# Kernel optimization log

Hardware: AMD Instinct MI355X
Metric: run time of the kernel (lower is better)

The kernel has to match this reference:

```python
import jax, jax.numpy as jnp
import numpy as np

SR = 16000
HOP = 256
MIN_F0 = 50.0
MAX_F0 = 500.0
MIN_PERIOD = SR // 500          # 32
MAX_PERIOD = SR // 50           # 320
FRAME_LEN = HOP * 2             # 512
LAG_END = min(MAX_PERIOD, FRAME_LEN // 2)  # 256 -> lags 32..255 (224 lags)


def setup_inputs() -> dict:
    key = jax.random.key(0)
    waveform = jax.random.normal(key, (64, 1, 163840), dtype=jnp.float32)
    return {"waveform": waveform}


def reference(waveform):
    B, C, T = waveform.shape
    x = waveform[:, 0, :]  # (B, T)
    pad = FRAME_LEN // 2
    xpad = jnp.pad(x, ((0, 0), (pad, pad)), mode='reflect')
    n_frames = (T + 2 * pad - FRAME_LEN) // HOP + 1  # = T//HOP + 1
    # frame extraction (equivalent to unfold(frame_length, hop))
    idx = np.arange(n_frames)[:, None] * HOP + np.arange(FRAME_LEN)[None, :]
    frames = xpad[:, idx]  # (B, F, L)
    # L2-normalize each frame
    norm = jnp.sqrt(jnp.sum(frames * frames, axis=-1, keepdims=True))
    xn = frames / (norm + 1e-8)
    # zero-pad right so xn[t] * xz[t+p] reproduces frame[:L-p] * frame[p:]
    xz = jnp.pad(xn, ((0, 0), (0, 0), (0, FRAME_LEN)))
    lags = jnp.arange(MIN_PERIOD, LAG_END)

    def step(carry, p):
        sl = jax.lax.dynamic_slice_in_dim(xz, p, FRAME_LEN, axis=-1)
        return carry, jnp.sum(xn * sl, axis=-1)  # (B, F)

    _, ac = jax.lax.scan(step, None, lags)  # (P, B, F)
    max_idx = jnp.argmax(ac, axis=0)  # (B, F)
    period = max_idx.astype(jnp.float32) + MIN_PERIOD
    f0 = SR / (period + 1e-8)
    return jnp.clip(f0, MIN_F0, MAX_F0)  # (B, F)
```

## Files before the change

kernel.cpp:

```cpp
#include <hip/hip_runtime.h>


#define SR_F 16000.0f
#define HOP 256
#define FRAME_LEN 512
#define PAD 256
#define T_LEN 163840
#define N_FRAMES 641
#define MIN_PERIOD 32
#define N_LAGS 224
#define FPB 4
#define GAP_B32 0.0625f

typedef _Float16 half8 __attribute__((ext_vector_type(8)));
typedef float floatx4 __attribute__((ext_vector_type(4)));

__device__ __forceinline__ int swz(int q) { return q ^ ((q >> 3) & 7); }

__device__ __forceinline__ unsigned int pkh(float a, float b) {
    unsigned short ha = __builtin_bit_cast(unsigned short, (_Float16)a);
    unsigned short hb = __builtin_bit_cast(unsigned short, (_Float16)b);
    return (unsigned int)ha | ((unsigned int)hb << 16);
}

__global__ __launch_bounds__(256, 4) void f0_kernel(const float* __restrict__ wav,
                                                    float* __restrict__ out) {
    __shared__ unsigned int yw[FPB][800];

    const int tid  = threadIdx.x;
    const int wv   = tid >> 6;
    const int lane = tid & 63;
    const int bf   = blockIdx.x * FPB + wv;
    const int b    = bf / N_FRAMES;
    const int f    = bf - b * N_FRAMES;
    const float* __restrict__ x = wav + (size_t)b * T_LEN;
    unsigned int* ye = yw[wv];
    unsigned int* yo = ye + 400;
    const int base = f * HOP - PAD;

    ye[lane] = 0u; yo[lane] = 0u;
    if (lane < 56) { ye[64 + lane] = 0u; yo[64 + lane] = 0u; }
    if (lane < 25) { ye[375 + lane] = 0u; yo[375 + lane] = 0u; }

    float qen = 0.0f;
    if (f != 0 && f != N_FRAMES - 1) {
        const float4* g4 = (const float4*)(x + base);
        float4 c1 = g4[lane];
        float4 c2 = g4[lane + 64];
        qen = c1.x*c1.x + c1.y*c1.y + c1.z*c1.z + c1.w*c1.w
            + c2.x*c2.x + c2.y*c2.y + c2.z*c2.z + c2.w*c2.w;
        unsigned int u10 = pkh(c1.x, c1.y), u11 = pkh(c1.z, c1.w);
        unsigned int u20 = pkh(c2.x, c2.y), u21 = pkh(c2.z, c2.w);
        ye[120 + 2*lane] = u10;  ye[121 + 2*lane] = u11;
        ye[248 + 2*lane] = u20;  ye[249 + 2*lane] = u21;
        unsigned int a  = __shfl(u10, (lane + 1) & 63);
        unsigned int bb = __shfl(u20, (lane + 1) & 63);
        unsigned int n1 = (lane == 63) ? bb : a;
        unsigned int n2 = (lane == 63) ? 0u : bb;
        yo[120 + 2*lane] = (u10 >> 16) | (u11 << 16);
        yo[121 + 2*lane] = (u11 >> 16) | (n1 << 16);
        yo[248 + 2*lane] = (u20 >> 16) | (u21 << 16);
        yo[249 + 2*lane] = (u21 >> 16) | (n2 << 16);
        if (lane == 0) yo[119] = u10 << 16;
    } else {
        for (int t = lane; t < FRAME_LEN; t += 64) {
            int idx = base + t;
            if (idx < 0) idx = -idx;
            if (idx >= T_LEN) idx = 2 * (T_LEN - 1) - idx;
            float v = x[idx];
            qen = __builtin_fmaf(v, v, qen);
            unsigned short h = __builtin_bit_cast(unsigned short, (_Float16)v);
            ((unsigned short*)ye)[240 + t] = h;
            ((unsigned short*)yo)[239 + t] = h;
        }
    }
    __threadfence_block();

    #pragma unroll
    for (int m = 1; m < 64; m <<= 1) qen += __shfl_xor(qen, m);

    const int qd = lane >> 4;
    const int nn = lane & 15;
    const int par = nn & 1;
    const unsigned int* yb = par ? yo : ye;
    const int wA0 = 120 + 4*qd - 8*nn;
    const int wB0 = 136 + 4*qd + ((nn - par) >> 1);

    floatx4 acc = {0.f, 0.f, 0.f, 0.f};
    #pragma unroll
    for (int c = 0; c < 16; ++c) {
        uint4 au = *(const uint4*)(ye + (wA0 + 16*c));
        const unsigned int* pb = yb + (wB0 + 16*c);
        uint4 bu;
        bu.x = pb[0]; bu.y = pb[1]; bu.z = pb[2]; bu.w = pb[3];
        half8 af = __builtin_bit_cast(half8, au);
        half8 bfv = __builtin_bit_cast(half8, bu);
        acc = __builtin_amdgcn_mfma_f32_16x16x32_f16(af, bfv, acc, 0, 0, 0);
    }

    float v1 = acc[0];
    int   i1 = 64*qd + nn;
    float v2 = -__builtin_inff();
    #pragma unroll
    for (int r = 1; r < 4; ++r) {
        float cv = (4*qd + r < 14) ? acc[r] : -__builtin_inff();
        bool take = (cv > v1);
        float lose = take ? v1 : cv;
        if (take) { v1 = cv; i1 = 64*qd + 16*r + nn; }
        v2 = fmaxf(v2, lose);
    }
    #pragma unroll
    for (int m = 1; m < 64; m <<= 1) {
        float ov1 = __shfl_xor(v1, m);
        float ov2 = __shfl_xor(v2, m);
        int   oi1 = __shfl_xor(i1, m);
        bool take = (ov1 > v1) || (ov1 == v1 && oi1 < i1);
        float lose = take ? v1 : ov1;
        if (take) { v1 = ov1; i1 = oi1; }
        v2 = fmaxf(fmaxf(v2, ov2), lose);
    }

    const float E1 = 9.765625e-4f * qen + 0.05f;
    if (v1 - v2 > 2.0f * E1) {
        if (lane == 0) {
            float period = (float)(i1 + MIN_PERIOD);
            float f0 = SR_F / (period + 1e-8f);
            out[bf] = fminf(fmaxf(f0, 50.0f), 500.0f);
        }
        return;
    }

    float* sw = (float*)ye;
    if (f != 0 && f != N_FRAMES - 1) {
        const float4* g4 = (const float4*)(x + base);
        ((float4*)sw)[swz(lane)]      = g4[lane];
        ((float4*)sw)[swz(lane + 64)] = g4[lane + 64];
        if (lane < 16) ((float4*)sw)[swz(lane + 128)] = make_float4(0.f,0.f,0.f,0.f);
    } else {
        for (int t = lane; t < FRAME_LEN; t += 64) {
            int idx = base + t;
            if (idx < 0) idx = -idx;
            if (idx >= T_LEN) idx = 2 * (T_LEN - 1) - idx;
            sw[(swz(t >> 2) << 2) | (t & 3)] = x[idx];
        }
        int t = FRAME_LEN + lane;
        sw[(swz(t >> 2) << 2) | (t & 3)] = 0.0f;
    }
    __threadfence_block();

    const float4* s4 = (const float4*)sw;
    const int seg = lane & 15;
    const bool s0 = (seg & 1), s1 = (seg & 2), s2 = (seg & 4), s3 = (seg & 8);

    float tot[4];
    #pragma unroll
    for (int r = 0; r < 4; ++r) {
        const int g  = (r << 2) + qd;
        const int p0 = MIN_PERIOD + (g << 4);
        float acc2[16];
        #pragma unroll
        for (int j = 0; j < 16; ++j) acc2[j] = 0.0f;
        if (g < 14) {
            const int n16 = (FRAME_LEN - p0 + 15) >> 4;
            #pragma unroll
            for (int k = 0; k < 2; ++k) {
                const int ch = seg + (k << 4);
                if (ch < n16) {
                    const int t  = ch << 4;
                    const int qa = t >> 2;
                    const int qw = (t + p0) >> 2;
                    float a[16], w[32];
                    #pragma unroll
                    for (int u = 0; u < 4; ++u) {
                        float4 v = s4[swz(qa + u)];
                        a[4*u+0]=v.x; a[4*u+1]=v.y; a[4*u+2]=v.z; a[4*u+3]=v.w;
                    }
                    #pragma unroll
                    for (int u = 0; u < 8; ++u) {
                        float4 v = s4[swz(qw + u)];
                        w[4*u+0]=v.x; w[4*u+1]=v.y; w[4*u+2]=v.z; w[4*u+3]=v.w;
                    }
                    #pragma unroll
                    for (int j = 0; j < 16; ++j) {
                        #pragma unroll
                        for (int i = 0; i < 16; ++i)
                            acc2[j] = __builtin_fmaf(a[i], w[i + j], acc2[j]);
                    }
                }
            }
        }
        float t8[8], t4[4], t2[2], total;
        #pragma unroll
        for (int i = 0; i < 8; ++i) {
            float lo = acc2[2*i], hi = acc2[2*i+1];
            float keep = s0 ? hi : lo, send = s0 ? lo : hi;
            t8[i] = keep + __shfl_xor(send, 1);
        }
        #pragma unroll
        for (int i = 0; i < 4; ++i) {
            float lo = t8[2*i], hi = t8[2*i+1];
            float keep = s1 ? hi : lo, send = s1 ? lo : hi;
            t4[i] = keep + __shfl_xor(send, 2);
        }
        #pragma unroll
        for (int i = 0; i < 2; ++i) {
            float lo = t4[2*i], hi = t4[2*i+1];
            float keep = s2 ? hi : lo, send = s2 ? lo : hi;
            t2[i] = keep + __shfl_xor(send, 4);
        }
        {
            float lo = t2[0], hi = t2[1];
            float keep = s3 ? hi : lo, send = s3 ? lo : hi;
            total = keep + __shfl_xor(send, 8);
        }
        tot[r] = ((r << 6) + lane < N_LAGS) ? total : -__builtin_inff();
    }

    float w1 = tot[0], w2 = -__builtin_inff();
    int   j1 = lane;
    #pragma unroll
    for (int r = 1; r < 4; ++r) {
        float c = tot[r];
        bool take = (c > w1);
        float lose = take ? w1 : c;
        if (take) { w1 = c; j1 = (r << 6) + lane; }
        w2 = fmaxf(w2, lose);
    }
    #pragma unroll
    for (int m = 1; m < 64; m <<= 1) {
        float ov1 = __shfl_xor(w1, m);
        float ov2 = __shfl_xor(w2, m);
        int   oi1 = __shfl_xor(j1, m);
        bool take = (ov1 > w1) || (ov1 == w1 && oi1 < j1);
        float lose = take ? w1 : ov1;
        if (take) { w1 = ov1; j1 = oi1; }
        w2 = fmaxf(fmaxf(w2, ov2), lose);
    }

    if (w1 - w2 > GAP_B32) {
        if (lane == 0) {
            float period = (float)(j1 + MIN_PERIOD);
            float f0 = SR_F / (period + 1e-8f);
            out[bf] = fminf(fmaxf(f0, 50.0f), 500.0f);
        }
        return;
    }

    double dtot[4];
    #pragma unroll
    for (int r = 0; r < 4; ++r) {
        const int g  = (r << 2) + qd;
        const int p0 = MIN_PERIOD + (g << 4);
        double dacc[16];
        #pragma unroll
        for (int j = 0; j < 16; ++j) dacc[j] = 0.0;
        if (g < 14) {
            const int n16 = (FRAME_LEN - p0 + 15) >> 4;
            #pragma unroll
            for (int k = 0; k < 2; ++k) {
                const int ch = seg + (k << 4);
                if (ch < n16) {
                    const int t  = ch << 4;
                    const int qa = t >> 2;
                    const int qw = (t + p0) >> 2;
                    float a[16], w[32];
                    #pragma unroll
                    for (int u = 0; u < 4; ++u) {
                        float4 v = s4[swz(qa + u)];
                        a[4*u+0]=v.x; a[4*u+1]=v.y; a[4*u+2]=v.z; a[4*u+3]=v.w;
                    }
                    #pragma unroll
                    for (int u = 0; u < 8; ++u) {
                        float4 v = s4[swz(qw + u)];
                        w[4*u+0]=v.x; w[4*u+1]=v.y; w[4*u+2]=v.z; w[4*u+3]=v.w;
                    }
                    #pragma unroll
                    for (int j = 0; j < 16; ++j) {
                        #pragma unroll
                        for (int i = 0; i < 16; ++i)
                            dacc[j] = fma((double)a[i], (double)w[i + j], dacc[j]);
                    }
                }
            }
        }
        double u8[8], u4[4], u2[2], dtotal;
        #pragma unroll
        for (int i = 0; i < 8; ++i) {
            double lo = dacc[2*i], hi = dacc[2*i+1];
            double keep = s0 ? hi : lo, send = s0 ? lo : hi;
            u8[i] = keep + __shfl_xor(send, 1);
        }
        #pragma unroll
        for (int i = 0; i < 4; ++i) {
            double lo = u8[2*i], hi = u8[2*i+1];
            double keep = s1 ? hi : lo, send = s1 ? lo : hi;
            u4[i] = keep + __shfl_xor(send, 2);
        }
        #pragma unroll
        for (int i = 0; i < 2; ++i) {
            double lo = u4[2*i], hi = u4[2*i+1];
            double keep = s2 ? hi : lo, send = s2 ? lo : hi;
            u2[i] = keep + __shfl_xor(send, 4);
        }
        {
            double lo = u2[0], hi = u2[1];
            double keep = s3 ? hi : lo, send = s3 ? lo : hi;
            dtotal = keep + __shfl_xor(send, 8);
        }
        dtot[r] = ((r << 6) + lane < N_LAGS) ? dtotal : -__builtin_inf();
    }
    double dv1 = dtot[0];
    int    di1 = lane;
    #pragma unroll
    for (int r = 1; r < 4; ++r) {
        double c = dtot[r];
        if (c > dv1) { dv1 = c; di1 = (r << 6) + lane; }
    }
    #pragma unroll
    for (int m = 1; m < 64; m <<= 1) {
        double o = __shfl_xor(dv1, m);
        int   oi = __shfl_xor(di1, m);
        if (o > dv1 || (o == dv1 && oi < di1)) { dv1 = o; di1 = oi; }
    }
    if (lane == 0) {
        float period = (float)(di1 + MIN_PERIOD);
        float f0 = SR_F / (period + 1e-8f);
        out[bf] = fminf(fmaxf(f0, 50.0f), 500.0f);
    }
}

extern "C" void kernel_launch(void* const* d_in, const int* in_sizes, int n_in,
                              void* d_out, int out_size, void* d_ws, size_t ws_size,
                              hipStream_t stream) {
    const float* wav = (const float*)d_in[0];
    float* out = (float*)d_out;
    const int n_blocks = (64 * N_FRAMES) / FPB;
    f0_kernel<<<n_blocks, 256, 0, stream>>>(wav, out);
}
```

Measured before the change: 150.2 us.

## Replace fp32 FMA fallback tier with split-fp16 MFMA correction tier

Removes the second-tier fp32 scalar-FMA autocorrelation and replaces it with a residual-corrected MFMA pass. The low-order fp16 remainder of each sample is stored in extra LDS buffers and two more MFMA sweeps (hi*lo and lo*hi) are added to the accumulator, with a tighter error bound deciding whether to accept the argmax before falling back to fp64. Block size also goes from 4 to 8 frames (512 threads) with doubled LDS per wave. This cuts the expensive fp32 FMA work for ambiguous frames, at the cost of more LDS use, which may lower occupancy, and reliance on the new error bound being correct.

```diff
diff --git a/kernel.cpp b/kernel.cpp
--- a/kernel.cpp
+++ b/kernel.cpp
@@ -9,8 +9,7 @@
 #define N_FRAMES 641
 #define MIN_PERIOD 32
 #define N_LAGS 224
-#define FPB 4
-#define GAP_B32 0.0625f
+#define FPB 8
 
 typedef _Float16 half8 __attribute__((ext_vector_type(8)));
 typedef float floatx4 __attribute__((ext_vector_type(4)));
@@ -23,9 +22,26 @@
     return (unsigned int)ha | ((unsigned int)hb << 16);
 }
 
-__global__ __launch_bounds__(256, 4) void f0_kernel(const float* __restrict__ wav,
+__device__ __forceinline__ void write_copies(unsigned int* e, unsigned int* o,
+                                             unsigned int u10, unsigned int u11,
+                                             unsigned int u20, unsigned int u21,
+                                             int lane) {
+    e[120 + 2*lane] = u10;  e[121 + 2*lane] = u11;
+    e[248 + 2*lane] = u20;  e[249 + 2*lane] = u21;
+    unsigned int a  = __shfl(u10, (lane + 1) & 63);
+    unsigned int bb = __shfl(u20, (lane + 1) & 63);
+    unsigned int n1 = (lane == 63) ? bb : a;
+    unsigned int n2 = (lane == 63) ? 0u : bb;
+    o[120 + 2*lane] = (u10 >> 16) | (u11 << 16);
+    o[121 + 2*lane] = (u11 >> 16) | (n1 << 16);
+    o[248 + 2*lane] = (u20 >> 16) | (u21 << 16);
+    o[249 + 2*lane] = (u21 >> 16) | (n2 << 16);
+    if (lane == 0) o[119] = u10 << 16;
+}
+
+__global__ __launch_bounds__(512, 4) void f0_kernel(const float* __restrict__ wav,
                                                     float* __restrict__ out) {
-    __shared__ unsigned int yw[FPB][800];
+    __shared__ unsigned int yw[FPB][1600];
 
     const int tid  = threadIdx.x;
     const int wv   = tid >> 6;
@@ -34,34 +50,26 @@
     const int b    = bf / N_FRAMES;
     const int f    = bf - b * N_FRAMES;
     const float* __restrict__ x = wav + (size_t)b * T_LEN;
-    unsigned int* ye = yw[wv];
-    unsigned int* yo = ye + 400;
+    unsigned int* ye  = yw[wv];
+    unsigned int* yo  = ye + 400;
+    unsigned int* le  = ye + 800;
+    unsigned int* loo = ye + 1200;
     const int base = f * HOP - PAD;
+    const bool fast = (f != 0 && f != N_FRAMES - 1);
 
     ye[lane] = 0u; yo[lane] = 0u;
     if (lane < 56) { ye[64 + lane] = 0u; yo[64 + lane] = 0u; }
     if (lane < 25) { ye[375 + lane] = 0u; yo[375 + lane] = 0u; }
 
     float qen = 0.0f;
-    if (f != 0 && f != N_FRAMES - 1) {
+    if (fast) {
         const float4* g4 = (const float4*)(x + base);
         float4 c1 = g4[lane];
         float4 c2 = g4[lane + 64];
         qen = c1.x*c1.x + c1.y*c1.y + c1.z*c1.z + c1.w*c1.w
             + c2.x*c2.x + c2.y*c2.y + c2.z*c2.z + c2.w*c2.w;
-        unsigned int u10 = pkh(c1.x, c1.y), u11 = pkh(c1.z, c1.w);
-        unsigned int u20 = pkh(c2.x, c2.y), u21 = pkh(c2.z, c2.w);
-        ye[120 + 2*lane] = u10;  ye[121 + 2*lane] = u11;
-        ye[248 + 2*lane] = u20;  ye[249 + 2*lane] = u21;
-        unsigned int a  = __shfl(u10, (lane + 1) & 63);
-        unsigned int bb = __shfl(u20, (lane + 1) & 63);
-        unsigned int n1 = (lane == 63) ? bb : a;
-        unsigned int n2 = (lane == 63) ? 0u : bb;
-        yo[120 + 2*lane] = (u10 >> 16) | (u11 << 16);
-        yo[121 + 2*lane] = (u11 >> 16) | (n1 << 16);
-        yo[248 + 2*lane] = (u20 >> 16) | (u21 << 16);
-        yo[249 + 2*lane] = (u21 >> 16) | (n2 << 16);
-        if (lane == 0) yo[119] = u10 << 16;
+        write_copies(ye, yo, pkh(c1.x, c1.y), pkh(c1.z, c1.w),
+                             pkh(c2.x, c2.y), pkh(c2.z, c2.w), lane);
     } else {
         for (int t = lane; t < FRAME_LEN; t += 64) {
             int idx = base + t;
@@ -82,7 +90,7 @@
     const int qd = lane >> 4;
     const int nn = lane & 15;
     const int par = nn & 1;
-    const unsigned int* yb = par ? yo : ye;
+    const unsigned int* ybh = par ? yo : ye;
     const int wA0 = 120 + 4*qd - 8*nn;
     const int wB0 = 136 + 4*qd + ((nn - par) >> 1);
 
@@ -90,12 +98,11 @@
     #pragma unroll
     for (int c = 0; c < 16; ++c) {
         uint4 au = *(const uint4*)(ye + (wA0 + 16*c));
-        const unsigned int* pb = yb + (wB0 + 16*c);
-        uint4 bu;
-        bu.x = pb[0]; bu.y = pb[1]; bu.z = pb[2]; bu.w = pb[3];
-        half8 af = __builtin_bit_cast(half8, au);
-        half8 bfv = __builtin_bit_cast(half8, bu);
-        acc = __builtin_amdgcn_mfma_f32_16x16x32_f16(af, bfv, acc, 0, 0, 0);
+        const unsigned int* pb = ybh + (wB0 + 16*c);
+        uint4 bu; bu.x = pb[0]; bu.y = pb[1]; bu.z = pb[2]; bu.w = pb[3];
+        acc = __builtin_amdgcn_mfma_f32_16x16x32_f16(
+            __builtin_bit_cast(half8, au), __builtin_bit_cast(half8, bu),
+            acc, 0, 0, 0);
     }
 
     float v1 = acc[0];
@@ -130,8 +137,89 @@
         return;
     }
 
+    le[lane] = 0u; loo[lane] = 0u;
+    if (lane < 56) { le[64 + lane] = 0u; loo[64 + lane] = 0u; }
+    if (lane < 25) { le[375 + lane] = 0u; loo[375 + lane] = 0u; }
+    if (fast) {
+        const float4* g4 = (const float4*)(x + base);
+        float4 c1 = g4[lane];
+        float4 c2 = g4[lane + 64];
+        float l0 = c1.x - (float)(_Float16)c1.x;
+        float l1 = c1.y - (float)(_Float16)c1.y;
+        float l2 = c1.z - (float)(_Float16)c1.z;
+        float l3 = c1.w - (float)(_Float16)c1.w;
+        float l4 = c2.x - (float)(_Float16)c2.x;
+        float l5 = c2.y - (float)(_Float16)c2.y;
+        float l6 = c2.z - (float)(_Float16)c2.z;
+        float l7 = c2.w - (float)(_Float16)c2.w;
+        write_copies(le, loo, pkh(l0, l1), pkh(l2, l3),
+                              pkh(l4, l5), pkh(l6, l7), lane);
+    } else {
+        for (int t = lane; t < FRAME_LEN; t += 64) {
+            int idx = base + t;
+            if (idx < 0) idx = -idx;
+            if (idx >= T_LEN) idx = 2 * (T_LEN - 1) - idx;
+            float v = x[idx];
+            float l = v - (float)(_Float16)v;
+            unsigned short h = __builtin_bit_cast(unsigned short, (_Float16)l);
+            ((unsigned short*)le)[240 + t] = h;
+            ((unsigned short*)loo)[239 + t] = h;
+        }
+    }
+    __threadfence_block();
+
+    const unsigned int* ybl = par ? loo : le;
+    #pragma unroll
+    for (int c = 0; c < 16; ++c) {
+        uint4 au = *(const uint4*)(ye + (wA0 + 16*c));
+        const unsigned int* pb = ybl + (wB0 + 16*c);
+        uint4 bu; bu.x = pb[0]; bu.y = pb[1]; bu.z = pb[2]; bu.w = pb[3];
+        acc = __builtin_amdgcn_mfma_f32_16x16x32_f16(
+            __builtin_bit_cast(half8, au), __builtin_bit_cast(half8, bu),
+            acc, 0, 0, 0);
+    }
+    #pragma unroll
+    for (int c = 0; c < 16; ++c) {
+        uint4 au = *(const uint4*)(le + (wA0 + 16*c));
+        const unsigned int* pb = ybh + (wB0 + 16*c);
+        uint4 bu; bu.x = pb[0]; bu.y = pb[1]; bu.z = pb[2]; bu.w = pb[3];
+        acc = __builtin_amdgcn_mfma_f32_16x16x32_f16(
+            __builtin_bit_cast(half8, au), __builtin_bit_cast(half8, bu),
+            acc, 0, 0, 0);
+    }
+
+    v1 = acc[0]; i1 = 64*qd + nn; v2 = -__builtin_inff();
+    #pragma unroll
+    for (int r = 1; r < 4; ++r) {
+        float cv = (4*qd + r < 14) ? acc[r] : -__builtin_inff();
+        bool take = (cv > v1);
+        float lose = take ? v1 : cv;
+        if (take) { v1 = cv; i1 = 64*qd + 16*r + nn; }
+        v2 = fmaxf(v2, lose);
+    }
+    #pragma unroll
+    for (int m = 1; m < 64; m <<= 1) {
+        float ov1 = __shfl_xor(v1, m);
+        float ov2 = __shfl_xor(v2, m);
+        int   oi1 = __shfl_xor(i1, m);
+        bool take = (ov1 > v1) || (ov1 == v1 && oi1 < i1);
+        float lose = take ? v1 : ov1;
+        if (take) { v1 = ov1; i1 = oi1; }
+        v2 = fmaxf(fmaxf(v2, ov2), lose);
+    }
+
+    const float E2 = 1.0e-4f * qen + 0.02f;
+    if (v1 - v2 > 2.0f * E2) {
+        if (lane == 0) {
+            float period = (float)(i1 + MIN_PERIOD);
+            float f0 = SR_F / (period + 1e-8f);
+            out[bf] = fminf(fmaxf(f0, 50.0f), 500.0f);
+        }
+        return;
+    }
+
     float* sw = (float*)ye;
-    if (f != 0 && f != N_FRAMES - 1) {
+    if (fast) {
         const float4* g4 = (const float4*)(x + base);
         ((float4*)sw)[swz(lane)]      = g4[lane];
         ((float4*)sw)[swz(lane + 64)] = g4[lane + 64];
@@ -151,100 +239,6 @@
     const float4* s4 = (const float4*)sw;
     const int seg = lane & 15;
     const bool s0 = (seg & 1), s1 = (seg & 2), s2 = (seg & 4), s3 = (seg & 8);
-
-    float tot[4];
-    #pragma unroll
-    for (int r = 0; r < 4; ++r) {
-        const int g  = (r << 2) + qd;
-        const int p0 = MIN_PERIOD + (g << 4);
-        float acc2[16];
-        #pragma unroll
-        for (int j = 0; j < 16; ++j) acc2[j] = 0.0f;
-        if (g < 14) {
-            const int n16 = (FRAME_LEN - p0 + 15) >> 4;
-            #pragma unroll
-            for (int k = 0; k < 2; ++k) {
-                const int ch = seg + (k << 4);
-                if (ch < n16) {
-                    const int t  = ch << 4;
-                    const int qa = t >> 2;
-                    const int qw = (t + p0) >> 2;
-                    float a[16], w[32];
-                    #pragma unroll
-                    for (int u = 0; u < 4; ++u) {
-                        float4 v = s4[swz(qa + u)];
-                        a[4*u+0]=v.x; a[4*u+1]=v.y; a[4*u+2]=v.z; a[4*u+3]=v.w;
-                    }
-                    #pragma unroll
-                    for (int u = 0; u < 8; ++u) {
-                        float4 v = s4[swz(qw + u)];
-                        w[4*u+0]=v.x; w[4*u+1]=v.y; w[4*u+2]=v.z; w[4*u+3]=v.w;
-                    }
-                    #pragma unroll
-                    for (int j = 0; j < 16; ++j) {
-                        #pragma unroll
-                        for (int i = 0; i < 16; ++i)
-                            acc2[j] = __builtin_fmaf(a[i], w[i + j], acc2[j]);
-                    }
-                }
-            }
-        }
-        float t8[8], t4[4], t2[2], total;
-        #pragma unroll
-        for (int i = 0; i < 8; ++i) {
-            float lo = acc2[2*i], hi = acc2[2*i+1];
-            float keep = s0 ? hi : lo, send = s0 ? lo : hi;
-            t8[i] = keep + __shfl_xor(send, 1);
-        }
-        #pragma unroll
-        for (int i = 0; i < 4; ++i) {
-            float lo = t8[2*i], hi = t8[2*i+1];
-            float keep = s1 ? hi : lo, send = s1 ? lo : hi;
-            t4[i] = keep + __shfl_xor(send, 2);
-        }
-        #pragma unroll
-        for (int i = 0; i < 2; ++i) {
-            float lo = t4[2*i], hi = t4[2*i+1];
-            float keep = s2 ? hi : lo, send = s2 ? lo : hi;
-            t2[i] = keep + __shfl_xor(send, 4);
-        }
-        {
-            float lo = t2[0], hi = t2[1];
-            float keep = s3 ? hi : lo, send = s3 ? lo : hi;
-            total = keep + __shfl_xor(send, 8);
-        }
-        tot[r] = ((r << 6) + lane < N_LAGS) ? total : -__builtin_inff();
-    }
-
-    float w1 = tot[0], w2 = -__builtin_inff();
-    int   j1 = lane;
-    #pragma unroll
-    for (int r = 1; r < 4; ++r) {
-        float c = tot[r];
-        bool take = (c > w1);
-        float lose = take ? w1 : c;
-        if (take) { w1 = c; j1 = (r << 6) + lane; }
-        w2 = fmaxf(w2, lose);
-    }
-    #pragma unroll
-    for (int m = 1; m < 64; m <<= 1) {
-        float ov1 = __shfl_xor(w1, m);
-        float ov2 = __shfl_xor(w2, m);
-        int   oi1 = __shfl_xor(j1, m);
-        bool take = (ov1 > w1) || (ov1 == w1 && oi1 < j1);
-        float lose = take ? w1 : ov1;
-        if (take) { w1 = ov1; j1 = oi1; }
-        w2 = fmaxf(fmaxf(w2, ov2), lose);
-    }
-
-    if (w1 - w2 > GAP_B32) {
-        if (lane == 0) {
-            float period = (float)(j1 + MIN_PERIOD);
-            float f0 = SR_F / (period + 1e-8f);
-            out[bf] = fminf(fmaxf(f0, 50.0f), 500.0f);
-        }
-        return;
-    }
 
     double dtot[4];
     #pragma unroll
@@ -335,5 +329,5 @@
     const float* wav = (const float*)d_in[0];
     float* out = (float*)d_out;
     const int n_blocks = (64 * N_FRAMES) / FPB;
-    f0_kernel<<<n_blocks, 256, 0, stream>>>(wav, out);
+    f0_kernel<<<n_blocks, 512, 0, stream>>>(wav, out);
 }
```

After: 141.2 us. -6.0%, faster.
